# Kernel tuning notes

Measured on AMD Instinct MI355X. Metric: run time of the kernel, lower is better.

## Reference

```python
import jax, jax.numpy as jnp
from jax import lax
import numpy as np

L, D, DM, E, DH, K, V, B, S = 4, 512, 128, 2, 128, 5, 50257, 2, 1024
EPS = 1e-6


def rmsnorm(x, w):
    return w * x * jax.lax.rsqrt(jnp.mean(x * x, axis=-1, keepdims=True) + EPS)


def rope(x):
    b, s, d = x.shape
    h = d // 2
    inv = 1.0 / (10000.0 ** (jnp.arange(h, dtype=jnp.float32) / h))
    freqs = jnp.arange(s, dtype=jnp.float32)[:, None] * inv[None, :]  # [S, h]
    emb = jnp.concatenate([freqs, freqs], axis=-1)  # [S, D]
    cos, sin = jnp.cos(emb)[None], jnp.sin(emb)[None]
    x1, x2 = x[..., :h], x[..., h:]
    rot = jnp.concatenate([-x2, x1], axis=-1)
    return x * cos + rot * sin


def causal_dwconv(x, w, b, dil):
    # x: [B,S,D]; w: [D,K] depthwise kernel; left-pad (K-1)*dil => causal.
    xc = jnp.transpose(x, (0, 2, 1))  # [B,D,S]
    k = w[:, None, :]  # [D,1,K]
    pad = (w.shape[-1] - 1) * dil
    y = lax.conv_general_dilated(xc, k, window_strides=(1,), padding=[(pad, 0)],
                                 rhs_dilation=(dil,),
                                 dimension_numbers=('NCH', 'OIH', 'NCH'),
                                 feature_group_count=x.shape[-1])
    return jnp.transpose(y, (0, 2, 1)) + b


def recurrence(x, win, bin_, wf, bf, wu, bu, wo, bo):
    # StructuredStateRecurrence: gated scan over time with memory dim DM.
    b_, s_, d_ = x.shape
    mu = jax.nn.silu(x @ win.T + bin_)            # [B,S,DM] silu(memory_proj_in)
    fx = x @ wf[:, :d_].T + bf                    # x-part of forget gate
    ux = x @ wu[:, :d_].T + bu                    # x-part of update gate
    ox = x @ wo[:, :d_].T + bo                    # x-part of output gate
    wfm, wum, wom = wf[:, d_:], wu[:, d_:], wo[:, d_:]

    def step(m, inp):
        fx_t, ux_t, mu_t, ox_t, x_t = inp
        f = jax.nn.sigmoid(fx_t + m @ wfm.T)
        u = jax.nn.sigmoid(ux_t + m @ wum.T)
        m = f * m + u * mu_t
        out = x_t + ox_t + m @ wom.T
        return m, out

    m0 = jnp.zeros((b_, DM), x.dtype)
    tr = lambda a: jnp.transpose(a, (1, 0, 2))
    m_final, ys = lax.scan(step, m0, (tr(fx), tr(ux), tr(mu), tr(ox), tr(x)))
    return jnp.transpose(ys, (1, 0, 2)), m_final


def setup_inputs() -> dict:
    key = jax.random.key(0)
    ks = iter(jax.random.split(key, 40))
    p = lambda shape, s=0.02: jax.random.normal(next(ks), shape, jnp.float32) * s
    return dict(
        tokens=jax.random.randint(next(ks), (B, S), 0, V),
        embed=p((V, D)),
        norm_w=jnp.ones((L, D)),
        dw_w=p((L, D, K), 0.1), dw_b=jnp.zeros((L, D)),
        pw_w=p((L, D, D)), pw_b=jnp.zeros((L, D)),
        rin_w=p((L, DM, D)), rin_b=jnp.zeros((L, DM)),
        rf_w=p((L, DM, D + DM)), rf_b=jnp.ones((L, DM)),
        ru_w=p((L, DM, D + DM)), ru_b=jnp.zeros((L, DM)),
        ro_w=p((L, D, D + DM)), ro_b=jnp.zeros((L, D)),
        rt_w=p((L, E, D)), rt_b=jnp.zeros((L, E)),
        e1_w=p((L, E, D, D)), e1_b=jnp.zeros((L, E, D)),
        e2_w=p((L, E, D, D)), e2_b=jnp.zeros((L, E, D)),
        fn_w=jnp.ones((L, D)),
        fd_w=p((L, DH, D)), fd_b=jnp.zeros((L, DH)),
        fu_w=p((L, D, DH)), fu_b=jnp.zeros((L, D)),
        final_norm_w=jnp.ones((D,)),
    )


def reference(tokens, embed, norm_w, dw_w, dw_b, pw_w, pw_b,
              rin_w, rin_b, rf_w, rf_b, ru_w, ru_b, ro_w, ro_b,
              rt_w, rt_b, e1_w, e1_b, e2_w, e2_b, fn_w,
              fd_w, fd_b, fu_w, fu_b, final_norm_w):
    dils = [max(1, int(np.exp(i * np.log(8) / L))) for i in range(L)]  # [1,1,2,4]
    x = embed[tokens]            # [B,S,D] token embedding
    x = rope(x)                  # rotary positional embedding (applied to full dim)
    for i in range(L):
        residual = x
        xn = rmsnorm(x, norm_w[i])
        # depthwise causal dilated conv + 1x1 pointwise conv
        xc = causal_dwconv(xn, dw_w[i], dw_b[i], dils[i])
        xc = xc @ pw_w[i].T + pw_b[i]
        # gated recurrent memory scan
        xr, _ = recurrence(xn, rin_w[i], rin_b[i], rf_w[i], rf_b[i],
                           ru_w[i], ru_b[i], ro_w[i], ro_b[i])
        h = xc + xr
        # EnhancedGatedFusion: softmax router over 2 dense experts
        r = jax.nn.softmax(h @ rt_w[i].T + rt_b[i], axis=-1)          # [B,S,E]
        hh = jax.nn.silu(jnp.einsum('bsd,eod->bseo', h, e1_w[i]) + e1_b[i])
        eo = jnp.einsum('bseo,epo->bsep', hh, e2_w[i]) + e2_b[i]      # [B,S,E,D]
        h = rmsnorm(h + jnp.einsum('bse,bsep->bsp', r, eo), fn_w[i])
        # LowRankFF: down -> GELU(exact) -> up
        h = h + (jax.nn.gelu(h @ fd_w[i].T + fd_b[i], approximate=False) @ fu_w[i].T + fu_b[i])
        x = h + residual
    x = rmsnorm(x, final_norm_w)
    logits = x @ embed.T          # tied output projection
    return logits
```

## Files before the change

kernel.cpp:

```cpp
#include <hip/hip_runtime.h>
#include <hip/hip_bf16.h>

#define Bsz 2
#define Ssz 1024
#define Dsz 512
#define DMs 128
#define Vsz 50257
#define ROWS (Bsz*Ssz)

typedef __attribute__((ext_vector_type(8))) short short8;
typedef __attribute__((ext_vector_type(4))) float f32x4;

#define DEV static __device__ __forceinline__

DEV unsigned short f2bf(float f){
  unsigned int u = __float_as_uint(f);
  unsigned int r = ((u >> 16) & 1u) + 0x7fffu;
  return (unsigned short)((u + r) >> 16);
}

__global__ __launch_bounds__(256) void k_embed_rope(
    const int* __restrict__ tokens, const float* __restrict__ embed, float* __restrict__ x)
{
  int row = blockIdx.x;
  int s = row & (Ssz-1);
  int t = threadIdx.x;
  int tok = tokens[row];
  const float* e = embed + (size_t)tok * Dsz;
  float e1 = e[t], e2 = e[t + 256];
  float inv = powf(10000.f, -(float)t * (1.f/256.f));
  float fr = (float)s * inv;
  float sn, cs;
  sincosf(fr, &sn, &cs);
  float* o = x + (size_t)row * Dsz;
  o[t]       = e1 * cs - e2 * sn;
  o[t + 256] = e2 * cs + e1 * sn;
}

__global__ __launch_bounds__(256) void k_rmsnorm(
    const float* __restrict__ a, const float* __restrict__ w, float* __restrict__ out)
{
  int row = blockIdx.x; int t = threadIdx.x;
  size_t base = (size_t)row * Dsz;
  float v0 = a[base + t];
  float v1 = a[base + t + 256];
  float ss = v0*v0 + v1*v1;
  #pragma unroll
  for (int off = 32; off > 0; off >>= 1) ss += __shfl_down(ss, off);
  __shared__ float sred[4];
  __shared__ float sscale;
  int wid = t >> 6, lane = t & 63;
  if (lane == 0) sred[wid] = ss;
  __syncthreads();
  if (t == 0) {
    float tot = sred[0] + sred[1] + sred[2] + sred[3];
    sscale = rsqrtf(tot * (1.f/Dsz) + 1e-6f);
  }
  __syncthreads();
  float sc = sscale;
  out[base + t]       = w[t]       * v0 * sc;
  out[base + t + 256] = w[t + 256] * v1 * sc;
}

__global__ __launch_bounds__(256) void k_combine_norm(
    const float* __restrict__ h, const float* __restrict__ e0,
    const float* __restrict__ e1, const float* __restrict__ rg,
    const float* __restrict__ w, float* __restrict__ out)
{
  int row = blockIdx.x; int t = threadIdx.x;
  size_t base = (size_t)row * Dsz;
  float r0 = rg[row*2], r1 = rg[row*2+1];
  float v0 = h[base + t]       + r0*e0[base + t]       + r1*e1[base + t];
  float v1 = h[base + t + 256] + r0*e0[base + t + 256] + r1*e1[base + t + 256];
  float ss = v0*v0 + v1*v1;
  #pragma unroll
  for (int off = 32; off > 0; off >>= 1) ss += __shfl_down(ss, off);
  __shared__ float sred[4];
  __shared__ float sscale;
  int wid = t >> 6, lane = t & 63;
  if (lane == 0) sred[wid] = ss;
  __syncthreads();
  if (t == 0) {
    float tot = sred[0] + sred[1] + sred[2] + sred[3];
    sscale = rsqrtf(tot * (1.f/Dsz) + 1e-6f);
  }
  __syncthreads();
  float sc = sscale;
  out[base + t]       = w[t]       * v0 * sc;
  out[base + t + 256] = w[t + 256] * v1 * sc;
}

__global__ __launch_bounds__(256) void k_dwconv(
    const float* __restrict__ xn, const float* __restrict__ w,
    const float* __restrict__ bias, float* __restrict__ out, int dil)
{
  int row = blockIdx.x;
  int b = row >> 10, s = row & (Ssz-1);
  int t = threadIdx.x;
  #pragma unroll
  for (int dd = 0; dd < 2; ++dd) {
    int d = t + dd*256;
    float acc = bias[d];
    #pragma unroll
    for (int j = 0; j < 5; ++j) {
      int sp = s - (4 - j) * dil;
      if (sp >= 0) acc += w[d*5 + j] * xn[((size_t)(b*Ssz + sp))*Dsz + d];
    }
    out[(size_t)row*Dsz + d] = acc;
  }
}

__global__ __launch_bounds__(256) void k_gemm128(
    const float* __restrict__ A, int lda,
    const float* __restrict__ B, int ldb,
    const float* __restrict__ bias,
    float* __restrict__ C, int ldc,
    int M, int N, int K)
{
  __shared__ __align__(16) unsigned short As[128][40];
  __shared__ __align__(16) unsigned short Bs[128][40];
  int t = threadIdx.x;
  int m0 = blockIdx.y * 128;
  int n0 = blockIdx.x * 128;
  int wid = t >> 6, lane = t & 63;
  int wr = wid >> 1, wc = wid & 1;
  f32x4 acc[4][4] = {};
  int tr = t >> 3;
  int tc = (t & 7) * 4;

  for (int k0 = 0; k0 < K; k0 += 32) {
    #pragma unroll
    for (int rr = 0; rr < 128; rr += 32) {
      int row = rr + tr;
      float4 av = *reinterpret_cast<const float4*>(A + (size_t)(m0 + row)*lda + k0 + tc);
      ushort4 ap; ap.x = f2bf(av.x); ap.y = f2bf(av.y); ap.z = f2bf(av.z); ap.w = f2bf(av.w);
      *reinterpret_cast<ushort4*>(&As[row][tc]) = ap;
      int bn = n0 + row;
      float4 bv = make_float4(0.f, 0.f, 0.f, 0.f);
      if (bn < N) bv = *reinterpret_cast<const float4*>(B + (size_t)bn*ldb + k0 + tc);
      ushort4 bp; bp.x = f2bf(bv.x); bp.y = f2bf(bv.y); bp.z = f2bf(bv.z); bp.w = f2bf(bv.w);
      *reinterpret_cast<ushort4*>(&Bs[row][tc]) = bp;
    }
    __syncthreads();
    int kc = (lane >> 4) * 8;
    int ra = lane & 15;
    short8 af[4], bf_[4];
    #pragma unroll
    for (int mt = 0; mt < 4; ++mt)
      af[mt] = *reinterpret_cast<const short8*>(&As[wr*64 + mt*16 + ra][kc]);
    #pragma unroll
    for (int nt = 0; nt < 4; ++nt)
      bf_[nt] = *reinterpret_cast<const short8*>(&Bs[wc*64 + nt*16 + ra][kc]);
    #pragma unroll
    for (int mt = 0; mt < 4; ++mt)
      #pragma unroll
      for (int nt = 0; nt < 4; ++nt)
        acc[mt][nt] = __builtin_amdgcn_mfma_f32_16x16x32_bf16(af[mt], bf_[nt], acc[mt][nt], 0, 0, 0);
    __syncthreads();
  }

  #pragma unroll
  for (int mt = 0; mt < 4; ++mt) {
    #pragma unroll
    for (int nt = 0; nt < 4; ++nt) {
      int n = n0 + wc*64 + nt*16 + (lane & 15);
      if (n >= N) continue;
      float bv = bias ? bias[n] : 0.f;
      #pragma unroll
      for (int j = 0; j < 4; ++j) {
        int m = m0 + wr*64 + mt*16 + (lane >> 4)*4 + j;
        C[(size_t)m*ldc + n] = acc[mt][nt][j] + bv;
      }
    }
  }
}

template<int OP, int NADD>
DEV void gemm64_body(unsigned short (*As)[40], unsigned short (*Bs)[40],
                     const float* __restrict__ A, int lda,
                     const float* __restrict__ B, int ldb,
                     const float* __restrict__ bias,
                     float* __restrict__ C, int ldc,
                     int K, int m0, int n0, int t,
                     const float* __restrict__ add1,
                     const float* __restrict__ add2,
                     const float* __restrict__ add3)
{
  int lane = t & 63;
  int wid = t >> 6;
  int wr = wid >> 1, wc = wid & 1;
  f32x4 acc[2][2] = {};
  int srow = t >> 2;
  int scb  = (t & 3) * 8;

  const float* apg = A + (size_t)(m0 + srow)*lda + scb;
  const float* bpg = B + (size_t)(n0 + srow)*ldb + scb;

  for (int k0 = 0; k0 < K; k0 += 32) {
    float4 a0 = *reinterpret_cast<const float4*>(apg + k0);
    float4 a1 = *reinterpret_cast<const float4*>(apg + k0 + 4);
    float4 b0 = *reinterpret_cast<const float4*>(bpg + k0);
    float4 b1 = *reinterpret_cast<const float4*>(bpg + k0 + 4);
    short8 av, bv;
    av[0]=f2bf(a0.x); av[1]=f2bf(a0.y); av[2]=f2bf(a0.z); av[3]=f2bf(a0.w);
    av[4]=f2bf(a1.x); av[5]=f2bf(a1.y); av[6]=f2bf(a1.z); av[7]=f2bf(a1.w);
    bv[0]=f2bf(b0.x); bv[1]=f2bf(b0.y); bv[2]=f2bf(b0.z); bv[3]=f2bf(b0.w);
    bv[4]=f2bf(b1.x); bv[5]=f2bf(b1.y); bv[6]=f2bf(b1.z); bv[7]=f2bf(b1.w);
    *reinterpret_cast<short8*>(&As[srow][scb]) = av;
    *reinterpret_cast<short8*>(&Bs[srow][scb]) = bv;
    __syncthreads();
    int kc = (lane >> 4) * 8;
    int ra = lane & 15;
    short8 af[2], bf_[2];
    #pragma unroll
    for (int mt = 0; mt < 2; ++mt)
      af[mt] = *reinterpret_cast<const short8*>(&As[wr*32 + mt*16 + ra][kc]);
    #pragma unroll
    for (int nt = 0; nt < 2; ++nt)
      bf_[nt] = *reinterpret_cast<const short8*>(&Bs[wc*32 + nt*16 + ra][kc]);
    #pragma unroll
    for (int mt = 0; mt < 2; ++mt)
      #pragma unroll
      for (int nt = 0; nt < 2; ++nt)
        acc[mt][nt] = __builtin_amdgcn_mfma_f32_16x16x32_bf16(af[mt], bf_[nt], acc[mt][nt], 0, 0, 0);
    __syncthreads();
  }

  #pragma unroll
  for (int mt = 0; mt < 2; ++mt) {
    #pragma unroll
    for (int nt = 0; nt < 2; ++nt) {
      int n = n0 + wc*32 + nt*16 + (lane & 15);
      float bv = bias ? bias[n] : 0.f;
      #pragma unroll
      for (int j = 0; j < 4; ++j) {
        int m = m0 + wr*32 + mt*16 + (lane >> 4)*4 + j;
        float v = acc[mt][nt][j] + bv;
        if (OP == 1) v = v / (1.f + expf(-v));
        else if (OP == 2) v = 0.5f * v * (1.f + erff(v * 0.70710678118f));
        size_t idx = (size_t)m*ldc + n;
        if (NADD >= 1) v += add1[idx];
        if (NADD >= 2) v += add2[idx];
        if (NADD >= 3) v += add3[idx];
        C[idx] = v;
      }
    }
  }
}

template<int OP, int NADD>
__global__ __launch_bounds__(256) void k_gemm64(
    const float* __restrict__ A, int lda,
    const float* __restrict__ B, int ldb,
    const float* __restrict__ bias,
    float* __restrict__ C, int ldc, int K,
    const float* add1, const float* add2, const float* add3)
{
  __shared__ __align__(16) unsigned short As[64][40];
  __shared__ __align__(16) unsigned short Bs[64][40];
  gemm64_body<OP,NADD>(As, Bs, A, lda, B, ldb, bias, C, ldc, K,
                       blockIdx.y*64, blockIdx.x*64, threadIdx.x, add1, add2, add3);
}

__global__ __launch_bounds__(256) void k_f2b(
    const float* __restrict__ in, unsigned short* __restrict__ o, int n8)
{
  int stride = gridDim.x * 256;
  for (int i = blockIdx.x*256 + threadIdx.x; i < n8; i += stride) {
    float4 a = reinterpret_cast<const float4*>(in)[i*2];
    float4 b = reinterpret_cast<const float4*>(in)[i*2+1];
    short8 v;
    v[0]=f2bf(a.x); v[1]=f2bf(a.y); v[2]=f2bf(a.z); v[3]=f2bf(a.w);
    v[4]=f2bf(b.x); v[5]=f2bf(b.y); v[6]=f2bf(b.z); v[7]=f2bf(b.w);
    *reinterpret_cast<short8*>(o + (size_t)i*8) = v;
  }
}

__global__ __launch_bounds__(256) void k_gemm_logits(
    const unsigned short* __restrict__ A, const unsigned short* __restrict__ B,
    float* __restrict__ C, int M, int N, int K)
{
  __shared__ __align__(16) unsigned short As[128][40];
  __shared__ __align__(16) unsigned short Bs[128][40];
  int t = threadIdx.x;
  int m0 = blockIdx.x * 128;
  int n0 = blockIdx.y * 128;
  int wid = t >> 6, lane = t & 63;
  int wr = wid >> 1, wc = wid & 1;
  f32x4 acc[4][4] = {};
  int srow = t >> 1;
  int scb  = (t & 1) * 16;

  const unsigned short* ap = A + (size_t)(m0 + srow)*K + scb;
  int bn = n0 + srow; if (bn >= N) bn = N - 1;
  const unsigned short* bp = B + (size_t)bn*K + scb;

  for (int k0 = 0; k0 < K; k0 += 32) {
    short8 a0 = *reinterpret_cast<const short8*>(ap + k0);
    short8 a1 = *reinterpret_cast<const short8*>(ap + k0 + 8);
    short8 b0 = *reinterpret_cast<const short8*>(bp + k0);
    short8 b1 = *reinterpret_cast<const short8*>(bp + k0 + 8);
    *reinterpret_cast<short8*>(&As[srow][scb])     = a0;
    *reinterpret_cast<short8*>(&As[srow][scb + 8]) = a1;
    *reinterpret_cast<short8*>(&Bs[srow][scb])     = b0;
    *reinterpret_cast<short8*>(&Bs[srow][scb + 8]) = b1;
    __syncthreads();
    int kc = (lane >> 4) * 8;
    int ra = lane & 15;
    short8 af[4], bf_[4];
    #pragma unroll
    for (int mt = 0; mt < 4; ++mt)
      af[mt] = *reinterpret_cast<const short8*>(&As[wr*64 + mt*16 + ra][kc]);
    #pragma unroll
    for (int nt = 0; nt < 4; ++nt)
      bf_[nt] = *reinterpret_cast<const short8*>(&Bs[wc*64 + nt*16 + ra][kc]);
    #pragma unroll
    for (int mt = 0; mt < 4; ++mt)
      #pragma unroll
      for (int nt = 0; nt < 4; ++nt)
        acc[mt][nt] = __builtin_amdgcn_mfma_f32_16x16x32_bf16(af[mt], bf_[nt], acc[mt][nt], 0, 0, 0);
    __syncthreads();
  }

  #pragma unroll
  for (int mt = 0; mt < 4; ++mt) {
    #pragma unroll
    for (int nt = 0; nt < 4; ++nt) {
      int n = n0 + wc*64 + nt*16 + (lane & 15);
      if (n >= N) continue;
      #pragma unroll
      for (int j = 0; j < 4; ++j) {
        int m = m0 + wr*64 + mt*16 + (lane >> 4)*4 + j;
        C[(size_t)m*N + n] = acc[mt][nt][j];
      }
    }
  }
}

__global__ __launch_bounds__(256, 2) void k_scan_fused(
    const float* __restrict__ rf_w, const float* __restrict__ ru_w,
    const float* __restrict__ fx, const float* __restrict__ ux,
    const float* __restrict__ mu, float* __restrict__ Mout,
    const float* __restrict__ g1A, const float* __restrict__ g1B, int g1ldb,
    const float* __restrict__ g1bias, float* __restrict__ g1C,
    const float* __restrict__ g2A, const float* __restrict__ g2B, int g2ldb,
    const float* __restrict__ g2bias, float* __restrict__ g2C)
{
  __shared__ __align__(16) unsigned short As[64][40];
  __shared__ __align__(16) unsigned short Bs[64][40];
  __shared__ __align__(16) unsigned short mb16[2][DMs];

  if (blockIdx.x >= 2) {
    int bid = blockIdx.x - 2;
    int which = bid >> 8;
    int idx = bid & 255;
    int n0 = (idx & 7) * 64;
    int m0 = (idx >> 3) * 64;
    if (which == 0)
      gemm64_body<0,0>(As, Bs, g1A, Dsz, g1B, g1ldb, g1bias, g1C, Dsz, Dsz, m0, n0, threadIdx.x, nullptr, nullptr, nullptr);
    else
      gemm64_body<0,0>(As, Bs, g2A, Dsz, g2B, g2ldb, g2bias, g2C, Dsz, Dsz, m0, n0, threadIdx.x, nullptr, nullptr, nullptr);
    return;
  }

  __builtin_amdgcn_s_setprio(1);

  int b = blockIdx.x;
  int t = threadIdx.x;
  int l = t & 63;
  int w = t >> 6;
  int g = l >> 4;
  int i16 = l & 15;

  short8 af[4][4];
  #pragma unroll
  for (int rt = 0; rt < 4; ++rt) {
    const float* src = (rt < 2 ? rf_w : ru_w) + (size_t)(w*32 + (rt&1)*16 + i16)*640 + 512;
    #pragma unroll
    for (int ks = 0; ks < 4; ++ks) {
      const float* p = src + ks*32 + g*8;
      float4 a = *reinterpret_cast<const float4*>(p);
      float4 c = *reinterpret_cast<const float4*>(p + 4);
      short8 v;
      v[0]=f2bf(a.x); v[1]=f2bf(a.y); v[2]=f2bf(a.z); v[3]=f2bf(a.w);
      v[4]=f2bf(c.x); v[5]=f2bf(c.y); v[6]=f2bf(c.z); v[7]=f2bf(c.w);
      af[rt][ks] = v;
    }
  }

  if (t < DMs) mb16[0][t] = 0;

  bool writer = (i16 & 4) == 0;
  int rho = ((i16 >> 3) << 4) + (g << 2) + (i16 & 3);
  int r = w*32 + rho;
  bool jb0 = (i16 & 1), jb1 = (i16 & 2), ab = (i16 & 8);

  const float* fxp = fx + (size_t)b*Ssz*DMs + r;
  const float* uxp = ux + (size_t)b*Ssz*DMs + r;
  const float* mup = mu + (size_t)b*Ssz*DMs + r;
  float* mo = Mout + (size_t)b*Ssz*DMs + r;
  float mreg = 0.f, fxv = 0.f, uxv = 0.f, muv = 0.f;
  __syncthreads();
  if (writer) { fxv = fxp[0]; uxv = uxp[0]; muv = mup[0]; }

  int cur = 0;
  for (int step = 0; step < Ssz; ++step) {
    short8 bf[4];
    #pragma unroll
    for (int ks = 0; ks < 4; ++ks)
      bf[ks] = *reinterpret_cast<const short8*>(&mb16[cur][ks*32 + g*8]);

    f32x4 zero = {0.f, 0.f, 0.f, 0.f};
    f32x4 a0 = zero, a1 = zero, a2 = zero, a3 = zero;
    #pragma unroll
    for (int ks = 0; ks < 4; ++ks) {
      a0 = __builtin_amdgcn_mfma_f32_16x16x32_bf16(af[0][ks], bf[ks], a0, 0, 0, 0);
      a1 = __builtin_amdgcn_mfma_f32_16x16x32_bf16(af[1][ks], bf[ks], a1, 0, 0, 0);
      a2 = __builtin_amdgcn_mfma_f32_16x16x32_bf16(af[2][ks], bf[ks], a2, 0, 0, 0);
      a3 = __builtin_amdgcn_mfma_f32_16x16x32_bf16(af[3][ks], bf[ks], a3, 0, 0, 0);
    }

    float f01 = jb0 ? a0[1] : a0[0];
    float f23 = jb0 ? a0[3] : a0[2];
    float fa0 = jb1 ? f23 : f01;
    float f01b = jb0 ? a1[1] : a1[0];
    float f23b = jb0 ? a1[3] : a1[2];
    float fa1 = jb1 ? f23b : f01b;
    float zf = ab ? fa1 : fa0;
    float u01 = jb0 ? a2[1] : a2[0];
    float u23 = jb0 ? a2[3] : a2[2];
    float ua0 = jb1 ? u23 : u01;
    float u01b = jb0 ? a3[1] : a3[0];
    float u23b = jb0 ? a3[3] : a3[2];
    float ua1 = jb1 ? u23b : u01b;
    float zu = ab ? ua1 : ua0;

    if (writer) {
      float f = __builtin_amdgcn_rcpf(1.f + __expf(-(zf + fxv)));
      float u = __builtin_amdgcn_rcpf(1.f + __expf(-(zu + uxv)));
      float mnew = f*mreg + u*muv;
      mreg = mnew;
      unsigned int pk;
      asm("v_cvt_pk_bf16_f32 %0, %1, %2" : "=v"(pk) : "v"(mnew), "v"(mnew));
      mb16[cur^1][r] = (unsigned short)pk;
      mo[(size_t)step*DMs] = mnew;
      if (step < Ssz-1) {
        fxv = fxp[(size_t)(step+1)*DMs];
        uxv = uxp[(size_t)(step+1)*DMs];
        muv = mup[(size_t)(step+1)*DMs];
      }
    }
    asm volatile("s_waitcnt lgkmcnt(0)\n\ts_barrier" ::: "memory");
    cur ^= 1;
  }
}

__global__ __launch_bounds__(64) void k_rt_softmax(
    const float* __restrict__ h, const float* __restrict__ rtw,
    const float* __restrict__ rtb, float* __restrict__ rg)
{
  int row = blockIdx.x; int lane = threadIdx.x;
  const float* hp = h + (size_t)row*Dsz;
  float a0 = 0.f, a1 = 0.f;
  #pragma unroll
  for (int k = lane; k < Dsz; k += 64) {
    float hv = hp[k];
    a0 += hv * rtw[k];
    a1 += hv * rtw[Dsz + k];
  }
  #pragma unroll
  for (int off = 32; off > 0; off >>= 1) {
    a0 += __shfl_down(a0, off);
    a1 += __shfl_down(a1, off);
  }
  if (lane == 0) {
    a0 += rtb[0]; a1 += rtb[1];
    float mx = fmaxf(a0, a1);
    float e0 = expf(a0 - mx), e1 = expf(a1 - mx);
    float s = e0 + e1;
    rg[row*2]     = e0 / s;
    rg[row*2 + 1] = e1 / s;
  }
}

extern "C" void kernel_launch(void* const* d_in, const int* in_sizes, int n_in,
                              void* d_out, int out_size, void* d_ws, size_t ws_size,
                              hipStream_t stream)
{
  const int*   tokens = (const int*)  d_in[0];
  const float* embed  = (const float*)d_in[1];
  const float* norm_w = (const float*)d_in[2];
  const float* dw_w   = (const float*)d_in[3];
  const float* dw_b   = (const float*)d_in[4];
  const float* pw_w   = (const float*)d_in[5];
  const float* pw_b   = (const float*)d_in[6];
  const float* rin_w  = (const float*)d_in[7];
  const float* rin_b  = (const float*)d_in[8];
  const float* rf_w   = (const float*)d_in[9];
  const float* rf_b   = (const float*)d_in[10];
  const float* ru_w   = (const float*)d_in[11];
  const float* ru_b   = (const float*)d_in[12];
  const float* ro_w   = (const float*)d_in[13];
  const float* ro_b   = (const float*)d_in[14];
  const float* rt_w   = (const float*)d_in[15];
  const float* rt_b   = (const float*)d_in[16];
  const float* e1_w   = (const float*)d_in[17];
  const float* e1_b   = (const float*)d_in[18];
  const float* e2_w   = (const float*)d_in[19];
  const float* e2_b   = (const float*)d_in[20];
  const float* fn_w   = (const float*)d_in[21];
  const float* fd_w   = (const float*)d_in[22];
  const float* fd_b   = (const float*)d_in[23];
  const float* fu_w   = (const float*)d_in[24];
  const float* fu_b   = (const float*)d_in[25];
  const float* fnorm  = (const float*)d_in[26];
  float* out = (float*)d_out;

  float* ws = (float*)d_ws;
  const size_t M1 = 1u << 20;
  float* x   = ws + 0*M1;
  float* xn  = ws + 1*M1;
  float* b2  = ws + 2*M1;
  float* b3  = ws + 3*M1;
  float* h   = ws + 4*M1;
  float* b5  = ws + 5*M1;
  float* mu  = ws + 7*M1;
  float* fx  = ws + 7*M1 + 262144;
  float* ux  = ws + 7*M1 + 2*262144;
  float* Mb  = ws + 7*M1 + 3*262144;
  float* g   = ws + 8*M1;
  float* rg  = ws + 8*M1 + 262144;
  const size_t EMB_ELEMS = (size_t)Vsz * Dsz;
  unsigned short* embb = (unsigned short*)(ws + 9*M1);
  bool big = ws_size >= (size_t)(9*M1*4) + EMB_ELEMS*2 + 1024;

  const int dils[4] = {1, 1, 2, 4};

  k_embed_rope<<<ROWS, 256, 0, stream>>>(tokens, embed, x);

  for (int i = 0; i < 4; ++i) {
    k_rmsnorm<<<ROWS,256,0,stream>>>(x, norm_w + i*Dsz, xn);
    k_dwconv<<<ROWS,256,0,stream>>>(xn, dw_w + i*Dsz*5, dw_b + i*Dsz, b2, dils[i]);
    {
      dim3 gr(DMs/64, ROWS/64);
      k_gemm64<1,0><<<gr,256,0,stream>>>(xn,Dsz, rin_w + (size_t)i*DMs*Dsz,Dsz, rin_b + i*DMs, mu,DMs, Dsz, nullptr,nullptr,nullptr);
      k_gemm64<0,0><<<gr,256,0,stream>>>(xn,Dsz, rf_w + (size_t)i*DMs*640,640, rf_b + i*DMs, fx,DMs, Dsz, nullptr,nullptr,nullptr);
      k_gemm64<0,0><<<gr,256,0,stream>>>(xn,Dsz, ru_w + (size_t)i*DMs*640,640, ru_b + i*DMs, ux,DMs, Dsz, nullptr,nullptr,nullptr);
    }
    k_scan_fused<<<2 + 512, 256, 0, stream>>>(
        rf_w + (size_t)i*DMs*640, ru_w + (size_t)i*DMs*640, fx, ux, mu, Mb,
        b2, pw_w + (size_t)i*Dsz*Dsz, Dsz, pw_b + i*Dsz, b3,
        xn, ro_w + (size_t)i*Dsz*640, 640, ro_b + i*Dsz, b5);
    {
      dim3 gr(Dsz/64, ROWS/64);
      k_gemm64<0,3><<<gr,256,0,stream>>>(Mb,DMs, ro_w + (size_t)i*Dsz*640 + 512,640, nullptr, h,Dsz, DMs, b3, xn, b5);
    }
    k_rt_softmax<<<ROWS,64,0,stream>>>(h, rt_w + i*2*Dsz, rt_b + i*2, rg);
    for (int e = 0; e < 2; ++e) {
      dim3 gr(Dsz/64, ROWS/64);
      k_gemm64<1,0><<<gr,256,0,stream>>>(h,Dsz, e1_w + (size_t)(i*2+e)*Dsz*Dsz,Dsz, e1_b + (i*2+e)*Dsz, b2,Dsz, Dsz, nullptr,nullptr,nullptr);
      k_gemm64<0,0><<<gr,256,0,stream>>>(b2,Dsz, e2_w + (size_t)(i*2+e)*Dsz*Dsz,Dsz, e2_b + (i*2+e)*Dsz, (e==0 ? b3 : b5),Dsz, Dsz, nullptr,nullptr,nullptr);
    }
    k_combine_norm<<<ROWS,256,0,stream>>>(h, b3, b5, rg, fn_w + i*Dsz, xn);
    {
      dim3 g1(DMs/64, ROWS/64), g2(Dsz/64, ROWS/64);
      k_gemm64<2,0><<<g1,256,0,stream>>>(xn,Dsz, fd_w + (size_t)i*DMs*Dsz,Dsz, fd_b + i*DMs, g,DMs, Dsz, nullptr,nullptr,nullptr);
      k_gemm64<0,2><<<g2,256,0,stream>>>(g,DMs, fu_w + (size_t)i*Dsz*DMs,DMs, fu_b + i*Dsz, x,Dsz, DMs, x, xn, nullptr);
    }
  }

  k_rmsnorm<<<ROWS,256,0,stream>>>(x, fnorm, xn);
  if (big) {
    unsigned short* xnb = (unsigned short*)b3;
    k_f2b<<<2048,256,0,stream>>>(embed, embb, (int)(EMB_ELEMS/8));
    k_f2b<<<512,256,0,stream>>>(xn, xnb, ROWS*Dsz/8);
    dim3 grid(ROWS/128, (Vsz + 127)/128);
    k_gemm_logits<<<grid,256,0,stream>>>(xnb, embb, out, ROWS, Vsz, Dsz);
  } else {
    dim3 grid((Vsz + 127)/128, ROWS/128);
    k_gemm128<<<grid,256,0,stream>>>(xn,Dsz, embed,Dsz, nullptr, out,Vsz, ROWS,Vsz,Dsz);
  }
}
```

Baseline: 2.417 ms.

## Batch projection and expert GEMMs, fuse final norm to bf16, swizzle logits grid

Folds the three recurrence input projections into one launch and the two experts' GEMMs into paired launches, which cuts launch count and lets the blocks run concurrently. The final rmsnorm now writes bf16 directly, removing a separate conversion pass. The logits GEMM remaps block indices so that consecutive blocks share embedding tiles for better L2 reuse. The scan loop is unrolled by two with fixed buffer indices. The expert path uses an extra workspace buffer, and the swizzle constant is hardcoded for this grid shape.

New measurement: 2.954 ms. 1.22x slower.

```diff
diff --git a/kernel.cpp b/kernel.cpp
--- a/kernel.cpp
+++ b/kernel.cpp
@@ -60,6 +60,31 @@
   float sc = sscale;
   out[base + t]       = w[t]       * v0 * sc;
   out[base + t + 256] = w[t + 256] * v1 * sc;
+}
+
+__global__ __launch_bounds__(256) void k_rmsnorm_b16(
+    const float* __restrict__ a, const float* __restrict__ w, unsigned short* __restrict__ out)
+{
+  int row = blockIdx.x; int t = threadIdx.x;
+  size_t base = (size_t)row * Dsz;
+  float v0 = a[base + t];
+  float v1 = a[base + t + 256];
+  float ss = v0*v0 + v1*v1;
+  #pragma unroll
+  for (int off = 32; off > 0; off >>= 1) ss += __shfl_down(ss, off);
+  __shared__ float sred[4];
+  __shared__ float sscale;
+  int wid = t >> 6, lane = t & 63;
+  if (lane == 0) sred[wid] = ss;
+  __syncthreads();
+  if (t == 0) {
+    float tot = sred[0] + sred[1] + sred[2] + sred[3];
+    sscale = rsqrtf(tot * (1.f/Dsz) + 1e-6f);
+  }
+  __syncthreads();
+  float sc = sscale;
+  out[base + t]       = f2bf(w[t]       * v0 * sc);
+  out[base + t + 256] = f2bf(w[t + 256] * v1 * sc);
 }
 
 __global__ __launch_bounds__(256) void k_combine_norm(
@@ -262,6 +287,42 @@
                        blockIdx.y*64, blockIdx.x*64, threadIdx.x, add1, add2, add3);
 }
 
+__global__ __launch_bounds__(256) void k_proj3(
+    const float* __restrict__ xn,
+    const float* __restrict__ rin_w, const float* __restrict__ rin_b,
+    const float* __restrict__ rf_w,  const float* __restrict__ rf_b,
+    const float* __restrict__ ru_w,  const float* __restrict__ ru_b,
+    float* __restrict__ mu, float* __restrict__ fx, float* __restrict__ ux)
+{
+  __shared__ __align__(16) unsigned short As[64][40];
+  __shared__ __align__(16) unsigned short Bs[64][40];
+  int which = blockIdx.x >> 1;
+  int n0 = (blockIdx.x & 1) * 64;
+  int m0 = blockIdx.y * 64;
+  if (which == 0)
+    gemm64_body<1,0>(As, Bs, xn, Dsz, rin_w, Dsz, rin_b, mu, DMs, Dsz, m0, n0, threadIdx.x, nullptr, nullptr, nullptr);
+  else if (which == 1)
+    gemm64_body<0,0>(As, Bs, xn, Dsz, rf_w, 640, rf_b, fx, DMs, Dsz, m0, n0, threadIdx.x, nullptr, nullptr, nullptr);
+  else
+    gemm64_body<0,0>(As, Bs, xn, Dsz, ru_w, 640, ru_b, ux, DMs, Dsz, m0, n0, threadIdx.x, nullptr, nullptr, nullptr);
+}
+
+template<int OP>
+__global__ __launch_bounds__(256) void k_expair(
+    const float* __restrict__ A0, const float* __restrict__ A1, int lda,
+    const float* __restrict__ B0, const float* __restrict__ B1, int ldb,
+    const float* __restrict__ bias0, const float* __restrict__ bias1,
+    float* __restrict__ C0, float* __restrict__ C1, int ldc, int K)
+{
+  __shared__ __align__(16) unsigned short As[64][40];
+  __shared__ __align__(16) unsigned short Bs[64][40];
+  int e = blockIdx.x >> 3;
+  int n0 = (blockIdx.x & 7) * 64;
+  gemm64_body<OP,0>(As, Bs, e ? A1 : A0, lda, e ? B1 : B0, ldb,
+                    e ? bias1 : bias0, e ? C1 : C0, ldc, K,
+                    blockIdx.y*64, n0, threadIdx.x, nullptr, nullptr, nullptr);
+}
+
 __global__ __launch_bounds__(256) void k_f2b(
     const float* __restrict__ in, unsigned short* __restrict__ o, int n8)
 {
@@ -283,8 +344,10 @@
   __shared__ __align__(16) unsigned short As[128][40];
   __shared__ __align__(16) unsigned short Bs[128][40];
   int t = threadIdx.x;
-  int m0 = blockIdx.x * 128;
-  int n0 = blockIdx.y * 128;
+  int lin = blockIdx.x + blockIdx.y * 16;
+  int swz = (lin & 7) * 786 + (lin >> 3);
+  int m0 = (swz & 15) * 128;
+  int n0 = (swz >> 4) * 128;
   int wid = t >> 6, lane = t & 63;
   int wr = wid >> 1, wc = wid & 1;
   f32x4 acc[4][4] = {};
@@ -403,12 +466,11 @@
   __syncthreads();
   if (writer) { fxv = fxp[0]; uxv = uxp[0]; muv = mup[0]; }
 
-  int cur = 0;
-  for (int step = 0; step < Ssz; ++step) {
+  auto scan_step = [&](int SRC, int DST, int step) __attribute__((always_inline)) {
     short8 bf[4];
     #pragma unroll
     for (int ks = 0; ks < 4; ++ks)
-      bf[ks] = *reinterpret_cast<const short8*>(&mb16[cur][ks*32 + g*8]);
+      bf[ks] = *reinterpret_cast<const short8*>(&mb16[SRC][ks*32 + g*8]);
 
     f32x4 zero = {0.f, 0.f, 0.f, 0.f};
     f32x4 a0 = zero, a1 = zero, a2 = zero, a3 = zero;
@@ -442,7 +504,7 @@
       mreg = mnew;
       unsigned int pk;
       asm("v_cvt_pk_bf16_f32 %0, %1, %2" : "=v"(pk) : "v"(mnew), "v"(mnew));
-      mb16[cur^1][r] = (unsigned short)pk;
+      mb16[DST][r] = (unsigned short)pk;
       mo[(size_t)step*DMs] = mnew;
       if (step < Ssz-1) {
         fxv = fxp[(size_t)(step+1)*DMs];
@@ -451,7 +513,11 @@
       }
     }
     asm volatile("s_waitcnt lgkmcnt(0)\n\ts_barrier" ::: "memory");
-    cur ^= 1;
+  };
+
+  for (int step = 0; step < Ssz; step += 2) {
+    scan_step(0, 1, step);
+    scan_step(1, 0, step + 1);
   }
 }
 
@@ -524,6 +590,7 @@
   float* b3  = ws + 3*M1;
   float* h   = ws + 4*M1;
   float* b5  = ws + 5*M1;
+  float* b6  = ws + 6*M1;
   float* mu  = ws + 7*M1;
   float* fx  = ws + 7*M1 + 262144;
   float* ux  = ws + 7*M1 + 2*262144;
@@ -542,10 +609,12 @@
     k_rmsnorm<<<ROWS,256,0,stream>>>(x, norm_w + i*Dsz, xn);
     k_dwconv<<<ROWS,256,0,stream>>>(xn, dw_w + i*Dsz*5, dw_b + i*Dsz, b2, dils[i]);
     {
-      dim3 gr(DMs/64, ROWS/64);
-      k_gemm64<1,0><<<gr,256,0,stream>>>(xn,Dsz, rin_w + (size_t)i*DMs*Dsz,Dsz, rin_b + i*DMs, mu,DMs, Dsz, nullptr,nullptr,nullptr);
-      k_gemm64<0,0><<<gr,256,0,stream>>>(xn,Dsz, rf_w + (size_t)i*DMs*640,640, rf_b + i*DMs, fx,DMs, Dsz, nullptr,nullptr,nullptr);
-      k_gemm64<0,0><<<gr,256,0,stream>>>(xn,Dsz, ru_w + (size_t)i*DMs*640,640, ru_b + i*DMs, ux,DMs, Dsz, nullptr,nullptr,nullptr);
+      dim3 gr(6, ROWS/64);
+      k_proj3<<<gr,256,0,stream>>>(xn,
+          rin_w + (size_t)i*DMs*Dsz, rin_b + i*DMs,
+          rf_w  + (size_t)i*DMs*640, rf_b  + i*DMs,
+          ru_w  + (size_t)i*DMs*640, ru_b  + i*DMs,
+          mu, fx, ux);
     }
     k_scan_fused<<<2 + 512, 256, 0, stream>>>(
         rf_w + (size_t)i*DMs*640, ru_w + (size_t)i*DMs*640, fx, ux, mu, Mb,
@@ -556,12 +625,18 @@
       k_gemm64<0,3><<<gr,256,0,stream>>>(Mb,DMs, ro_w + (size_t)i*Dsz*640 + 512,640, nullptr, h,Dsz, DMs, b3, xn, b5);
     }
     k_rt_softmax<<<ROWS,64,0,stream>>>(h, rt_w + i*2*Dsz, rt_b + i*2, rg);
-    for (int e = 0; e < 2; ++e) {
-      dim3 gr(Dsz/64, ROWS/64);
-      k_gemm64<1,0><<<gr,256,0,stream>>>(h,Dsz, e1_w + (size_t)(i*2+e)*Dsz*Dsz,Dsz, e1_b + (i*2+e)*Dsz, b2,Dsz, Dsz, nullptr,nullptr,nullptr);
-      k_gemm64<0,0><<<gr,256,0,stream>>>(b2,Dsz, e2_w + (size_t)(i*2+e)*Dsz*Dsz,Dsz, e2_b + (i*2+e)*Dsz, (e==0 ? b3 : b5),Dsz, Dsz, nullptr,nullptr,nullptr);
-    }
-    k_combine_norm<<<ROWS,256,0,stream>>>(h, b3, b5, rg, fn_w + i*Dsz, xn);
+    {
+      dim3 ge(16, ROWS/64);
+      k_expair<1><<<ge,256,0,stream>>>(h, h, Dsz,
+          e1_w + (size_t)(i*2+0)*Dsz*Dsz, e1_w + (size_t)(i*2+1)*Dsz*Dsz, Dsz,
+          e1_b + (i*2+0)*Dsz, e1_b + (i*2+1)*Dsz,
+          b2, b5, Dsz, Dsz);
+      k_expair<0><<<ge,256,0,stream>>>(b2, b5, Dsz,
+          e2_w + (size_t)(i*2+0)*Dsz*Dsz, e2_w + (size_t)(i*2+1)*Dsz*Dsz, Dsz,
+          e2_b + (i*2+0)*Dsz, e2_b + (i*2+1)*Dsz,
+          b3, b6, Dsz, Dsz);
+    }
+    k_combine_norm<<<ROWS,256,0,stream>>>(h, b3, b6, rg, fn_w + i*Dsz, xn);
     {
       dim3 g1(DMs/64, ROWS/64), g2(Dsz/64, ROWS/64);
       k_gemm64<2,0><<<g1,256,0,stream>>>(xn,Dsz, fd_w + (size_t)i*DMs*Dsz,Dsz, fd_b + i*DMs, g,DMs, Dsz, nullptr,nullptr,nullptr);
@@ -569,14 +644,14 @@
     }
   }
 
-  k_rmsnorm<<<ROWS,256,0,stream>>>(x, fnorm, xn);
   if (big) {
     unsigned short* xnb = (unsigned short*)b3;
+    k_rmsnorm_b16<<<ROWS,256,0,stream>>>(x, fnorm, xnb);
     k_f2b<<<2048,256,0,stream>>>(embed, embb, (int)(EMB_ELEMS/8));
-    k_f2b<<<512,256,0,stream>>>(xn, xnb, ROWS*Dsz/8);
     dim3 grid(ROWS/128, (Vsz + 127)/128);
     k_gemm_logits<<<grid,256,0,stream>>>(xnb, embb, out, ROWS, Vsz, Dsz);
   } else {
+    k_rmsnorm<<<ROWS,256,0,stream>>>(x, fnorm, xn);
     dim3 grid((Vsz + 127)/128, ROWS/128);
     k_gemm128<<<grid,256,0,stream>>>(xn,Dsz, embed,Dsz, nullptr, out,Vsz, ROWS,Vsz,Dsz);
   }
```
